# Performance work log

Hardware: AMD Instinct MI355X
Metric: run time of the kernel (lower is better)

## Reference

```python
import jax, jax.numpy as jnp
import numpy as np


def setup_inputs() -> dict:
    key = jax.random.key(0)
    k0, k1, k2, k3, k4 = jax.random.split(key, 5)
    K, LENGTH, D, B, MAXDEPTH = 50000, 65536, 128, 1024, 16
    weights = jax.random.normal(k0, (LENGTH, D), dtype=jnp.float32)
    x = jax.random.normal(k1, (B, D), dtype=jnp.float32)
    y = jax.random.randint(k2, (B,), 0, K, dtype=jnp.int64)
    # padded per-class paths of internal (pseudo-class) nodes; real paths index [K, LENGTH)
    path_idx = jax.random.randint(k3, (K, MAXDEPTH), 0, LENGTH, dtype=jnp.int64)
    path_len = jax.random.randint(k4, (K,), 0, MAXDEPTH, dtype=jnp.int32)
    return {"weights": weights, "x": x, "y": y, "path_idx": path_idx, "path_len": path_len}


def reference(weights, x, y, path_idx, path_len):
    # weights: [LENGTH, d]; x: [B, d]; y: [B]; path_idx: [K, Dmax]; path_len: [K]
    K, Dmax = path_idx.shape
    # mask out padded path slots (original loops over len(path)-1 real ancestors)
    mask = (jnp.arange(Dmax)[None, :] < path_len[:, None]).astype(weights.dtype)  # [K, Dmax]
    # gather ancestor rows and sum along the path; add the class's own row j
    path_sum = jnp.einsum("kpd,kp->kd", weights[path_idx], mask)  # [K, d]
    added_weights = weights[:K] + path_sum                        # [K, d]
    logits = x @ added_weights.T                                  # [B, K]
    logp = jax.nn.log_softmax(logits, axis=-1)
    loss = -jnp.take_along_axis(logp, y[:, None], axis=1).mean()  # CrossEntropyLoss (mean)
    return loss, logits, added_weights
```

## Files before the change

### kernel.cpp

```cpp
#include <hip/hip_runtime.h>
#include <math.h>

#define KCLS  50000
#define KP    50048
#define DIM   128
#define BATCH 1024
#define MAXD  16

typedef __attribute__((ext_vector_type(8))) short short8;
typedef __attribute__((ext_vector_type(4))) float floatx4;

__device__ __forceinline__ unsigned short f2bf(float f) {
    unsigned u = __float_as_uint(f);
    u += 0x7fffu + ((u >> 16) & 1u);
    return (unsigned short)(u >> 16);
}

__global__ __launch_bounds__(256) void aw_kernel(
    const float* __restrict__ weights, const int* __restrict__ path_idx,
    const int* __restrict__ path_len, float* __restrict__ aw,
    unsigned short* __restrict__ awb)
{
    int t = threadIdx.x;
    int c = t >> 5;
    int lane = t & 31;
    int k = blockIdx.x * 8 + c;
    int col = lane * 4;

    if (k >= KCLS) {
        ushort4 z = {0, 0, 0, 0};
        *(ushort4*)(awb + (size_t)k * DIM + col) = z;
        return;
    }

    float4 acc = *(const float4*)(weights + (size_t)k * DIM + col);
    int len = path_len[k];
    const int* pp = path_idx + (size_t)k * MAXD;
    for (int p = 0; p < len; ++p) {
        int idx = pp[p];
        float4 wv = *(const float4*)(weights + (size_t)idx * DIM + col);
        acc.x += wv.x; acc.y += wv.y; acc.z += wv.z; acc.w += wv.w;
    }
    *(float4*)(aw + (size_t)k * DIM + col) = acc;
    ushort4 hv = { f2bf(acc.x), f2bf(acc.y), f2bf(acc.z), f2bf(acc.w) };
    *(ushort4*)(awb + (size_t)k * DIM + col) = hv;
}

__global__ __launch_bounds__(256) void xconv_kernel(
    const float* __restrict__ x, unsigned short* __restrict__ xb)
{
    int i = (blockIdx.x * 256 + threadIdx.x) * 4;
    float4 v = *(const float4*)(x + i);
    ushort4 hv = { f2bf(v.x), f2bf(v.y), f2bf(v.z), f2bf(v.w) };
    *(ushort4*)(xb + i) = hv;
}

__global__ __launch_bounds__(256) void gemm_kernel(
    const unsigned short* __restrict__ Xb,
    const unsigned short* __restrict__ Wb,
    float* __restrict__ logits)
{
    int tid = threadIdx.x;
    int wave = tid >> 6, lane = tid & 63;
    int r = lane & 15, quad = lane >> 4;
    int m0 = blockIdx.y * 128 + (wave >> 1) * 64;
    int n0 = blockIdx.x * 128 + (wave & 1) * 64;

    const unsigned short* ap = Xb + (size_t)(m0 + r) * DIM + quad * 8;
    const unsigned short* bp = Wb + (size_t)(n0 + r) * DIM + quad * 8;

    floatx4 acc[4][4];
    #pragma unroll
    for (int i = 0; i < 4; ++i)
        #pragma unroll
        for (int j = 0; j < 4; ++j)
            acc[i][j] = (floatx4){0.f, 0.f, 0.f, 0.f};

    #pragma unroll
    for (int kk = 0; kk < 4; ++kk) {
        short8 a[4], b[4];
        #pragma unroll
        for (int i = 0; i < 4; ++i)
            a[i] = *(const short8*)(ap + (size_t)(i * 16) * DIM + kk * 32);
        #pragma unroll
        for (int j = 0; j < 4; ++j)
            b[j] = *(const short8*)(bp + (size_t)(j * 16) * DIM + kk * 32);
        #pragma unroll
        for (int i = 0; i < 4; ++i)
            #pragma unroll
            for (int j = 0; j < 4; ++j)
                acc[i][j] = __builtin_amdgcn_mfma_f32_16x16x32_bf16(
                    a[i], b[j], acc[i][j], 0, 0, 0);
    }

    #pragma unroll
    for (int i = 0; i < 4; ++i) {
        int mrow = m0 + i * 16 + quad * 4;
        #pragma unroll
        for (int j = 0; j < 4; ++j) {
            int col = n0 + j * 16 + r;
            if (col < KCLS) {
                float* cp = logits + (size_t)mrow * KCLS + col;
                #pragma unroll
                for (int reg = 0; reg < 4; ++reg)
                    cp[(size_t)reg * KCLS] = acc[i][j][reg];
            }
        }
    }
}

__global__ __launch_bounds__(256) void lse_kernel(
    const float* __restrict__ logits, const int* __restrict__ y,
    float* __restrict__ loss)
{
    int b = blockIdx.x;
    const float* row = logits + (size_t)b * KCLS;
    float m = -INFINITY, s = 0.f;

    auto upd = [&](float v) {
        if (v <= m) {
            s += __expf(v - m);
        } else {
            s = s * __expf(m - v) + 1.f;
            m = v;
        }
    };

    if (threadIdx.x < 3) upd(row[threadIdx.x]);
    const float4* rv = (const float4*)(row + 3);
    for (int i = threadIdx.x; i < 12499; i += 256) {
        float4 v = rv[i];
        upd(v.x); upd(v.y); upd(v.z); upd(v.w);
    }
    if (threadIdx.x == 3) upd(row[49999]);

    #pragma unroll
    for (int off = 32; off > 0; off >>= 1) {
        float m2 = __shfl_down(m, off);
        float s2 = __shfl_down(s, off);
        float M = fmaxf(m, m2);
        s = s * __expf(m - M) + s2 * __expf(m2 - M);
        m = M;
    }
    __shared__ float sm[4], ss[4];
    int w = threadIdx.x >> 6, l = threadIdx.x & 63;
    if (l == 0) { sm[w] = m; ss[w] = s; }
    __syncthreads();
    if (threadIdx.x == 0) {
        m = sm[0]; s = ss[0];
        #pragma unroll
        for (int i = 1; i < 4; ++i) {
            float M = fmaxf(m, sm[i]);
            s = s * __expf(m - M) + ss[i] * __expf(sm[i] - M);
            m = M;
        }
        float lse = m + __logf(s);
        float ly = row[y[b]];
        atomicAdd(loss, (lse - ly) * (1.0f / BATCH));
    }
}

extern "C" void kernel_launch(void* const* d_in, const int* in_sizes, int n_in,
                              void* d_out, int out_size, void* d_ws, size_t ws_size,
                              hipStream_t stream)
{
    const float* weights  = (const float*)d_in[0];
    const float* x        = (const float*)d_in[1];
    const int*   y        = (const int*)d_in[2];
    const int*   path_idx = (const int*)d_in[3];
    const int*   path_len = (const int*)d_in[4];

    float* out    = (float*)d_out;
    float* loss   = out;
    float* logits = out + 1;
    float* aw     = out + 1 + (size_t)BATCH * KCLS;

    unsigned short* awb = (unsigned short*)d_ws;
    unsigned short* xb  = awb + (size_t)KP * DIM;

    hipMemsetAsync(loss, 0, sizeof(float), stream);

    aw_kernel<<<KP / 8, 256, 0, stream>>>(weights, path_idx, path_len, aw, awb);
    xconv_kernel<<<BATCH * DIM / 1024, 256, 0, stream>>>(x, xb);

    gemm_kernel<<<dim3(KP / 128, BATCH / 128), 256, 0, stream>>>(xb, awb, logits);

    lse_kernel<<<BATCH, 256, 0, stream>>>(logits, y, loss);
}
```

Baseline: 388.9 us.

## Fuse per-tile log-sum-exp partials into GEMM epilogue and add small finalize kernel

The GEMM epilogue now computes a per-row max and sum-exp over its 128-column tile, using lane shuffles and shared memory, and writes one (max, sum) pair per row per tile into a workspace buffer. A small finalize kernel merges the 391 partials per row and reads only the target logit. This avoids re-reading the full 200 MB logits matrix in a separate log-sum-exp pass. The cost is extra shuffle and exp work in the GEMM epilogue plus a block-wide sync.

Result: slower. 415.2 us (+6.8%).

```diff
diff --git a/kernel.cpp b/kernel.cpp
--- a/kernel.cpp
+++ b/kernel.cpp
@@ -3,6 +3,8 @@
 
 #define KCLS  50000
 #define KP    50048
+#define NBLK  (KP / 128)
+#define NSTR  392
 #define DIM   128
 #define BATCH 1024
 #define MAXD  16
@@ -58,7 +60,8 @@
 __global__ __launch_bounds__(256) void gemm_kernel(
     const unsigned short* __restrict__ Xb,
     const unsigned short* __restrict__ Wb,
-    float* __restrict__ logits)
+    float* __restrict__ logits,
+    float2* __restrict__ partials)
 {
     int tid = threadIdx.x;
     int wave = tid >> 6, lane = tid & 63;
@@ -107,33 +110,61 @@
             }
         }
     }
-}
-
-__global__ __launch_bounds__(256) void lse_kernel(
-    const float* __restrict__ logits, const int* __restrict__ y,
-    float* __restrict__ loss)
+
+    bool ok[4];
+    #pragma unroll
+    for (int j = 0; j < 4; ++j) ok[j] = (n0 + j * 16 + r) < KCLS;
+
+    __shared__ float2 part[128][2];
+    int halfn = wave & 1;
+    int rowbase = (wave >> 1) * 64;
+
+    #pragma unroll
+    for (int i = 0; i < 4; ++i) {
+        #pragma unroll
+        for (int reg = 0; reg < 4; ++reg) {
+            float v0 = ok[0] ? acc[i][0][reg] : -INFINITY;
+            float v1 = ok[1] ? acc[i][1][reg] : -INFINITY;
+            float v2 = ok[2] ? acc[i][2][reg] : -INFINITY;
+            float v3 = ok[3] ? acc[i][3][reg] : -INFINITY;
+            float m = fmaxf(fmaxf(v0, v1), fmaxf(v2, v3));
+            #pragma unroll
+            for (int msk = 1; msk < 16; msk <<= 1)
+                m = fmaxf(m, __shfl_xor(m, msk));
+            float s = __expf(v0 - m) + __expf(v1 - m)
+                    + __expf(v2 - m) + __expf(v3 - m);
+            #pragma unroll
+            for (int msk = 1; msk < 16; msk <<= 1)
+                s += __shfl_xor(s, msk);
+            if (r == 0)
+                part[rowbase + i * 16 + quad * 4 + reg][halfn] = make_float2(m, s);
+        }
+    }
+    __syncthreads();
+
+    if (tid < 128) {
+        float2 p0 = part[tid][0];
+        float2 p1 = part[tid][1];
+        float M = fmaxf(p0.x, p1.x);
+        float S = p0.y * __expf(p0.x - M) + p1.y * __expf(p1.x - M);
+        partials[(size_t)(blockIdx.y * 128 + tid) * NSTR + blockIdx.x]
+            = make_float2(M, S);
+    }
+}
+
+__global__ __launch_bounds__(64) void finalize_kernel(
+    const float2* __restrict__ partials, const float* __restrict__ logits,
+    const int* __restrict__ y, float* __restrict__ loss)
 {
     int b = blockIdx.x;
-    const float* row = logits + (size_t)b * KCLS;
+    const float2* row = partials + (size_t)b * NSTR;
     float m = -INFINITY, s = 0.f;
-
-    auto upd = [&](float v) {
-        if (v <= m) {
-            s += __expf(v - m);
-        } else {
-            s = s * __expf(m - v) + 1.f;
-            m = v;
-        }
-    };
-
-    if (threadIdx.x < 3) upd(row[threadIdx.x]);
-    const float4* rv = (const float4*)(row + 3);
-    for (int i = threadIdx.x; i < 12499; i += 256) {
-        float4 v = rv[i];
-        upd(v.x); upd(v.y); upd(v.z); upd(v.w);
-    }
-    if (threadIdx.x == 3) upd(row[49999]);
-
+    for (int i = threadIdx.x; i < NBLK; i += 64) {
+        float2 p = row[i];
+        float M = fmaxf(m, p.x);
+        s = s * __expf(m - M) + p.y * __expf(p.x - M);
+        m = M;
+    }
     #pragma unroll
     for (int off = 32; off > 0; off >>= 1) {
         float m2 = __shfl_down(m, off);
@@ -142,20 +173,9 @@
         s = s * __expf(m - M) + s2 * __expf(m2 - M);
         m = M;
     }
-    __shared__ float sm[4], ss[4];
-    int w = threadIdx.x >> 6, l = threadIdx.x & 63;
-    if (l == 0) { sm[w] = m; ss[w] = s; }
-    __syncthreads();
     if (threadIdx.x == 0) {
-        m = sm[0]; s = ss[0];
-        #pragma unroll
-        for (int i = 1; i < 4; ++i) {
-            float M = fmaxf(m, sm[i]);
-            s = s * __expf(m - M) + ss[i] * __expf(sm[i] - M);
-            m = M;
-        }
         float lse = m + __logf(s);
-        float ly = row[y[b]];
+        float ly = logits[(size_t)b * KCLS + y[b]];
         atomicAdd(loss, (lse - ly) * (1.0f / BATCH));
     }
 }
@@ -177,13 +197,14 @@
 
     unsigned short* awb = (unsigned short*)d_ws;
     unsigned short* xb  = awb + (size_t)KP * DIM;
+    float2* partials = (float2*)(xb + (size_t)BATCH * DIM);
 
     hipMemsetAsync(loss, 0, sizeof(float), stream);
 
     aw_kernel<<<KP / 8, 256, 0, stream>>>(weights, path_idx, path_len, aw, awb);
     xconv_kernel<<<BATCH * DIM / 1024, 256, 0, stream>>>(x, xb);
 
-    gemm_kernel<<<dim3(KP / 128, BATCH / 128), 256, 0, stream>>>(xb, awb, logits);
-
-    lse_kernel<<<BATCH, 256, 0, stream>>>(logits, y, loss);
-}
+    gemm_kernel<<<dim3(NBLK, BATCH / 128), 256, 0, stream>>>(xb, awb, logits, partials);
+
+    finalize_kernel<<<BATCH, 64, 0, stream>>>(partials, logits, y, loss);
+}
```
